# Kernel optimization log

Hardware: AMD Instinct MI355X
Metric: run time of the kernel (lower is better)

## Reference

```python
import jax, jax.numpy as jnp
import numpy as np

B, S, H, STATIC = 128, 128, 256, 2
BLOCKS = S // 2            # rotate_types = 2 for block_dim=2, allow_rot=True
DYN = 3 * BLOCKS           # dynamic channels: move / rotate_small / rotate_large


def setup_inputs() -> dict:
    key = jax.random.key(0)
    ks = jax.random.split(key, 16)
    p = lambda k, shape: (jax.random.normal(k, shape, jnp.float32) * 0.1)
    return {
        "static": jax.random.normal(ks[0], (B, STATIC + 1, S), jnp.float32),
        "dynamic": jnp.zeros((B, DYN, S), jnp.float32),
        "decoder_input": jax.random.normal(ks[1], (B, STATIC, 1), jnp.float32),
        # static/dynamic/decoder 1x1 conv encoders (weight [H, C_in], bias [H])
        "enc_s_W": p(ks[2], (H, STATIC)), "enc_s_b": p(ks[3], (H,)),
        "enc_d_W": p(ks[4], (H, DYN)),    "enc_d_b": p(ks[5], (H,)),
        "dec_W": p(ks[6], (H, STATIC)),   "dec_b": p(ks[7], (H,)),
        # single-layer GRU (torch layout: [3H, H] gates r,z,n)
        "gru_W_ih": p(ks[8], (3 * H, H)), "gru_W_hh": p(ks[9], (3 * H, H)),
        "gru_b_ih": p(ks[10], (3 * H,)),  "gru_b_hh": p(ks[11], (3 * H,)),
        # encoder attention and pointer heads: v [H], W [H, 3H]
        "attn_v": p(ks[12], (H,)), "attn_W": p(ks[13], (H, 3 * H)),
        "ptr_v": p(ks[14], (H,)),  "ptr_W": p(ks[15], (H, 3 * H)),
    }


def reference(static, dynamic, decoder_input,
              enc_s_W, enc_s_b, enc_d_W, enc_d_b, dec_W, dec_b,
              gru_W_ih, gru_W_hh, gru_b_ih, gru_b_hh,
              attn_v, attn_W, ptr_v, ptr_W):
    static_part = static[:, 1:, :]                                  # [B, STATIC, S]
    static_h = jnp.einsum('hi,bis->bhs', enc_s_W, static_part) + enc_s_b[None, :, None]
    dynamic_h = jnp.einsum('hi,bis->bhs', enc_d_W, dynamic) + enc_d_b[None, :, None]

    # initial mask from dynamic state (move + rotate feasibility)
    bn = dynamic.shape[1] // 3
    move = dynamic[:, :bn, :].sum(1)
    dyn_mask = dynamic[:, bn:2 * bn, :].sum(1) * dynamic[:, 2 * bn:3 * bn, :].sum(1) + move
    logmask = jnp.where(dyn_mask != 0, -jnp.inf, 0.0)               # log(current_mask), [B, S]

    hsz = gru_W_hh.shape[1]
    h0 = jnp.zeros((static.shape[0], hsz), static.dtype)            # GRU default zero state

    def gru_cell(x, h):
        gi = x @ gru_W_ih.T + gru_b_ih
        gh = h @ gru_W_hh.T + gru_b_hh
        ir, iz, inn = jnp.split(gi, 3, -1)
        hr, hz, hn = jnp.split(gh, 3, -1)
        r = jax.nn.sigmoid(ir + hr)
        z = jax.nn.sigmoid(iz + hz)
        n = jnp.tanh(inn + r * hn)
        return (1.0 - z) * n + z * h

    def step(carry, _):
        h_prev, dec_in = carry
        dec_h = jnp.einsum('hi,bi->bh', dec_W, dec_in[:, :, 0]) + dec_b   # decoder 1x1 conv
        h = gru_cell(dec_h, h_prev)                                       # rnn_out == new hidden
        rnn_b = jnp.broadcast_to(h[:, :, None], static_h.shape)
        hid = jnp.concatenate([static_h, dynamic_h, rnn_b], axis=1)       # [B, 3H, S]
        attn = jax.nn.softmax(
            jnp.einsum('h,bhs->bs', attn_v,
                       jnp.tanh(jnp.einsum('hk,bks->bhs', attn_W, hid))), axis=-1)
        context = jnp.einsum('bs,bhs->bh', attn, static_h)
        ctx_b = jnp.broadcast_to(context[:, :, None], static_h.shape)
        energy = jnp.concatenate([static_h, dynamic_h, ctx_b], axis=1)    # [B, 3H, S]
        logits = jnp.einsum('h,bhs->bs', ptr_v,
                            jnp.tanh(jnp.einsum('hk,bks->bhs', ptr_W, energy)))
        probs = jax.nn.softmax(logits + logmask, axis=-1)                 # [B, S]
        ptr = jnp.argmax(probs, axis=1)                                   # greedy (eval mode)
        logp = jnp.log(jnp.max(probs, axis=1))
        new_dec = jax.lax.stop_gradient(
            jnp.take_along_axis(static_part, ptr[:, None, None], axis=2))  # [B, STATIC, 1]
        return (h, new_dec), (ptr, logp)

    (_, _), (ptrs, logps) = jax.lax.scan(step, (h0, decoder_input), None,
                                         length=static_part.shape[2])
    tour_idx = ptrs.T    # [B, S]
    tour_logp = logps.T  # [B, S]
    return tour_idx, tour_logp
```

## Files before the change

kernel.cpp:

```cpp
#include <hip/hip_runtime.h>
#include <hip/hip_bf16.h>
#include <math.h>

#define BB   128
#define SS   128
#define HH   256
#define DYNN 192
#define LC   96

#define OFF_FLAG  0
#define OFF_G     64
#define OFF_G0    (OFF_G + 1536)
#define OFF_M1A   (OFF_G0 + 768)
#define OFF_CA    (OFF_M1A + 512)
#define OFF_M1P   (OFF_CA + 256)
#define OFF_CP    (OFF_M1P + 512)
#define OFF_M3P   (OFF_CP + 256)
#define OFF_CP3   (OFF_M3P + 512)
#define OFF_LM    (OFF_CP3 + 256)
#define OFF_M2A   (OFF_LM + 16384)
#define OFF_M2P   (OFF_M2A + 49152)
#define OFF_BASEA (OFF_M2P + 49152)
#define OFF_BASEP (OFF_BASEA + 4194304)
#define OFF_END   (OFF_BASEP + 4194304)

__device__ __forceinline__ float tanh_fast(float x) {
    float e = __builtin_amdgcn_exp2f(x * 2.885390081777927f);
    return 1.0f - 2.0f * __builtin_amdgcn_rcpf(e + 1.0f);
}

__device__ __forceinline__ void ybar(int* cnt, bool arrive, int target) {
    if (arrive && (threadIdx.x & 63) == 0)
        __hip_atomic_fetch_add(cnt, 1, __ATOMIC_RELEASE, __HIP_MEMORY_SCOPE_WORKGROUP);
    while (__hip_atomic_load(cnt, __ATOMIC_ACQUIRE, __HIP_MEMORY_SCOPE_WORKGROUP) < target)
        __builtin_amdgcn_s_sleep(1);
}

__global__ void k1_logmask(const float* __restrict__ dyn, float* __restrict__ lm,
                           int* __restrict__ flag) {
    int g = blockIdx.x * 256 + threadIdx.x;
    if (g >= BB * SS) return;
    int b = g >> 7, s = g & 127;
    const float* p = dyn + (size_t)b * DYNN * SS + s;
    float mv = 0.f, m1 = 0.f, m2 = 0.f;
    bool nz = false;
    for (int i = 0; i < 64; ++i)        { float v = p[(size_t)i * SS]; mv += v; nz |= (v != 0.f); }
    for (int i = 64; i < 128; ++i)      { float v = p[(size_t)i * SS]; m1 += v; nz |= (v != 0.f); }
    for (int i = 128; i < 192; ++i)     { float v = p[(size_t)i * SS]; m2 += v; nz |= (v != 0.f); }
    float dm = m1 * m2 + mv;
    lm[g] = (dm != 0.f) ? -__builtin_inff() : 0.f;
    if (nz) atomicOr(flag, 1);
}

__global__ void k0a_folds(const float* __restrict__ Wih, const float* __restrict__ bih,
                          const float* __restrict__ dW,  const float* __restrict__ db,
                          const float* __restrict__ aW,  const float* __restrict__ pW,
                          const float* __restrict__ esW, const float* __restrict__ esb,
                          const float* __restrict__ edb, float* __restrict__ wsf) {
    int idx = blockIdx.x * 256 + threadIdx.x;
    float* G   = wsf + OFF_G;
    float* g0  = wsf + OFF_G0;
    float* M1a = wsf + OFF_M1A;
    float* ca  = wsf + OFF_CA;
    float* M1p = wsf + OFF_M1P;
    float* cp  = wsf + OFF_CP;
    float* M3p = wsf + OFF_M3P;
    float* cp3 = wsf + OFF_CP3;
    if (idx < 1536) {
        int r = idx >> 1, j = idx & 1;
        float a = 0.f;
        for (int k = 0; k < 256; ++k) a += Wih[r * 256 + k] * dW[k * 2 + j];
        G[idx] = a;
    } else if (idx < 2304) {
        int r = idx - 1536;
        float a = 0.f;
        for (int k = 0; k < 256; ++k) a += Wih[r * 256 + k] * db[k];
        g0[r] = a + bih[r];
    } else if (idx < 2816) {
        int t = idx - 2304; int h = t >> 1, j = t & 1;
        float a = 0.f;
        for (int k = 0; k < 256; ++k) a += aW[h * 768 + k] * esW[k * 2 + j];
        M1a[t] = a;
    } else if (idx < 3072) {
        int h = idx - 2816;
        float a = 0.f, b2 = 0.f;
        for (int k = 0; k < 256; ++k) a  += aW[h * 768 + k]       * esb[k];
        for (int k = 0; k < 256; ++k) b2 += aW[h * 768 + 256 + k] * edb[k];
        ca[h] = a + b2;
    } else if (idx < 3584) {
        int t = idx - 3072; int h = t >> 1, j = t & 1;
        float a = 0.f;
        for (int k = 0; k < 256; ++k) a += pW[h * 768 + k] * esW[k * 2 + j];
        M1p[t] = a;
    } else if (idx < 3840) {
        int h = idx - 3584;
        float a = 0.f, b2 = 0.f;
        for (int k = 0; k < 256; ++k) a  += pW[h * 768 + k]       * esb[k];
        for (int k = 0; k < 256; ++k) b2 += pW[h * 768 + 256 + k] * edb[k];
        cp[h] = a + b2;
    } else if (idx < 4352) {
        int t = idx - 3840; int h = t >> 1, j = t & 1;
        float a = 0.f;
        for (int k = 0; k < 256; ++k) a += pW[h * 768 + 512 + k] * esW[k * 2 + j];
        M3p[t] = a;
    } else if (idx < 4608) {
        int h = idx - 4352;
        float a = 0.f;
        for (int k = 0; k < 256; ++k) a += pW[h * 768 + 512 + k] * esb[k];
        cp3[h] = a;
    }
}

__global__ void k0b_m2(const float* __restrict__ aW, const float* __restrict__ pW,
                       const float* __restrict__ edW, float* __restrict__ wsf,
                       const int* __restrict__ flag) {
    if (*flag == 0) return;
    int idx = blockIdx.x * 256 + threadIdx.x;
    if (idx >= 2 * 49152) return;
    int which = idx / 49152;
    int t = idx % 49152;
    int h = t / DYNN, i = t % DYNN;
    const float* W = which ? pW : aW;
    float a = 0.f;
    for (int k = 0; k < 256; ++k) a += W[h * 768 + 256 + k] * edW[k * DYNN + i];
    wsf[(which ? OFF_M2P : OFF_M2A) + t] = a;
}

__global__ void k2_bases(const float* __restrict__ stat, const float* __restrict__ dyn,
                         float* __restrict__ wsf, const int* __restrict__ flag) {
    if (*flag == 0) return;
    __shared__ float col[DYNN];
    __shared__ float s01[2];
    const float* M1a = wsf + OFF_M1A; const float* ca  = wsf + OFF_CA;
    const float* M1p = wsf + OFF_M1P; const float* cp  = wsf + OFF_CP;
    const float* M2a = wsf + OFF_M2A; const float* M2p = wsf + OFF_M2P;
    float* basea = wsf + OFF_BASEA;   float* basep = wsf + OFF_BASEP;
    for (int pair = blockIdx.x; pair < BB * SS; pair += gridDim.x) {
        int b = pair >> 7, s = pair & 127;
        if (threadIdx.x < DYNN) col[threadIdx.x] = dyn[((size_t)b * DYNN + threadIdx.x) * SS + s];
        if (threadIdx.x == DYNN) {
            s01[0] = stat[((size_t)b * 3 + 1) * SS + s];
            s01[1] = stat[((size_t)b * 3 + 2) * SS + s];
        }
        __syncthreads();
        int h = threadIdx.x;
        float aa = fmaf(M1a[h * 2], s01[0], fmaf(M1a[h * 2 + 1], s01[1], ca[h]));
        float pp = fmaf(M1p[h * 2], s01[0], fmaf(M1p[h * 2 + 1], s01[1], cp[h]));
        for (int i = 0; i < DYNN; ++i) {
            aa = fmaf(M2a[h * DYNN + i], col[i], aa);
            pp = fmaf(M2p[h * DYNN + i], col[i], pp);
        }
        basea[((size_t)b * SS + s) * HH + h] = aa;
        basep[((size_t)b * SS + s) * HH + h] = pp;
        __syncthreads();
    }
}

__global__ __launch_bounds__(1024) void k3_seq(
    const float* __restrict__ stat, const float* __restrict__ dec_inp,
    const float* __restrict__ Whh, const float* __restrict__ bhh_g,
    const float* __restrict__ aW, const float* __restrict__ av,
    const float* __restrict__ pv, const float* __restrict__ wsf,
    int allow_general, float* __restrict__ out) {
    const int b = blockIdx.x;
    const int tid = threadIdx.x;

    __shared__ float sh_whh[LC][256];
    __shared__ float sh_gh[768], sh_hv[256], sh_t1[256], sh_a[128];
    __shared__ float sh_sp0[128], sh_sp1[128], sh_lm[128];
    __shared__ float4 qa1[64], qa2[64], qva[64];
    __shared__ float4 qp1[64], qp2[64], qvp[64];
    __shared__ float sh_M3p[512];
    __shared__ float sh_ca[256], sh_cp[256], sh_cp3[256];
    __shared__ float sh_G[1536], sh_g0[768], sh_bhh[768];
    __shared__ float sh_va[256], sh_vp[256];
    __shared__ float sh_scal[4];
    __shared__ int ycnt;

    const float* G_   = wsf + OFF_G;   const float* g0_  = wsf + OFF_G0;
    const float* M1a_ = wsf + OFF_M1A; const float* ca_  = wsf + OFF_CA;
    const float* M1p_ = wsf + OFF_M1P; const float* cp_  = wsf + OFF_CP;
    const float* M3p_ = wsf + OFF_M3P; const float* cp3_ = wsf + OFF_CP3;
    const float* lm_  = wsf + OFF_LM;
    const float* basea = wsf + OFF_BASEA;
    const float* basep = wsf + OFF_BASEP;
    const int* flag = (const int*)wsf;

    {
        float4* dst = (float4*)&sh_whh[0][0];
        const float4* src = (const float4*)Whh;
        for (int i = tid; i < LC * 64; i += 1024) dst[i] = src[i];
    }
    for (int i = tid; i < 1536; i += 1024) sh_G[i] = G_[i];
    for (int i = tid; i < 768; i += 1024) {
        sh_g0[i] = g0_[i];
        float bv = bhh_g[i];
        sh_bhh[i] = bv;
        sh_gh[i] = bv;
    }
    for (int i = tid; i < 512; i += 1024) sh_M3p[i] = M3p_[i];
    for (int i = tid; i < 256; i += 1024) {
        sh_ca[i] = ca_[i]; sh_cp[i] = cp_[i]; sh_cp3[i] = cp3_[i];
        sh_va[i] = av[i];  sh_vp[i] = pv[i];  sh_hv[i] = 0.f;
    }
    for (int i = tid; i < 128; i += 1024) {
        sh_sp0[i] = stat[((size_t)b * 3 + 1) * SS + i];
        sh_sp1[i] = stat[((size_t)b * 3 + 2) * SS + i];
        sh_lm[i]  = lm_[b * SS + i];
    }
    if (tid < 64) {
        int q = tid;
        qa1[q] = make_float4(M1a_[(4*q+0)*2], M1a_[(4*q+1)*2], M1a_[(4*q+2)*2], M1a_[(4*q+3)*2]);
        qa2[q] = make_float4(M1a_[(4*q+0)*2+1], M1a_[(4*q+1)*2+1], M1a_[(4*q+2)*2+1], M1a_[(4*q+3)*2+1]);
        qva[q] = make_float4(av[4*q+0], av[4*q+1], av[4*q+2], av[4*q+3]);
    } else if (tid < 128) {
        int q = tid - 64;
        qp1[q] = make_float4(M1p_[(4*q+0)*2], M1p_[(4*q+1)*2], M1p_[(4*q+2)*2], M1p_[(4*q+3)*2]);
        qp2[q] = make_float4(M1p_[(4*q+0)*2+1], M1p_[(4*q+1)*2+1], M1p_[(4*q+2)*2+1], M1p_[(4*q+3)*2+1]);
        qvp[q] = make_float4(pv[4*q+0], pv[4*q+1], pv[4*q+2], pv[4*q+3]);
    }
    if (tid == 0) {
        sh_scal[0] = dec_inp[b * 2 + 0];
        sh_scal[1] = dec_inp[b * 2 + 1];
        ycnt = 0;
    }
    const bool dz = (!allow_general) || (*flag == 0);
    __syncthreads();

    for (int t = 0; t < SS; ++t) {
        if (tid < 256) {
            int k = tid;
            float d0 = sh_scal[0], d1 = sh_scal[1];
            float gr = fmaf(sh_G[k * 2],          d0, fmaf(sh_G[k * 2 + 1],          d1, sh_g0[k]));
            float gz = fmaf(sh_G[(k + 256) * 2],  d0, fmaf(sh_G[(k + 256) * 2 + 1],  d1, sh_g0[k + 256]));
            float gn = fmaf(sh_G[(k + 512) * 2],  d0, fmaf(sh_G[(k + 512) * 2 + 1],  d1, sh_g0[k + 512]));
            float r = 1.f / (1.f + expf(-(gr + sh_gh[k])));
            float z = 1.f / (1.f + expf(-(gz + sh_gh[k + 256])));
            float n = tanhf(gn + r * sh_gh[k + 512]);
            sh_hv[k] = (1.f - z) * n + z * sh_hv[k];
        }
        __syncthreads();

        if (tid < 512) {
            if (t + 1 < SS) {
                const int xg = tid >> 4, xj = tid & 15;
                float4 hx0 = ((const float4*)sh_hv)[xj];
                float4 hx1 = ((const float4*)sh_hv)[xj + 16];
                float4 hx2 = ((const float4*)sh_hv)[xj + 32];
                float4 hx3 = ((const float4*)sh_hv)[xj + 48];
                #pragma unroll
                for (int k = 0; k < 3; ++k) {
                    int r = xg + 32 * k;
                    const float4* Wr = (const float4*)&sh_whh[r][0];
                    float4 w0 = Wr[xj];
                    float4 w1 = Wr[xj + 16];
                    float4 w2 = Wr[xj + 32];
                    float4 w3 = Wr[xj + 48];
                    float acc = 0.f;
                    acc = fmaf(w0.x, hx0.x, fmaf(w0.y, hx0.y, fmaf(w0.z, hx0.z, fmaf(w0.w, hx0.w, acc))));
                    acc = fmaf(w1.x, hx1.x, fmaf(w1.y, hx1.y, fmaf(w1.z, hx1.z, fmaf(w1.w, hx1.w, acc))));
                    acc = fmaf(w2.x, hx2.x, fmaf(w2.y, hx2.y, fmaf(w2.z, hx2.z, fmaf(w2.w, hx2.w, acc))));
                    acc = fmaf(w3.x, hx3.x, fmaf(w3.y, hx3.y, fmaf(w3.z, hx3.z, fmaf(w3.w, hx3.w, acc))));
                    acc += __shfl_xor(acc, 1, 16); acc += __shfl_xor(acc, 2, 16);
                    acc += __shfl_xor(acc, 4, 16); acc += __shfl_xor(acc, 8, 16);
                    if (xj == 0) sh_gh[r] = acc + sh_bhh[r];
                }
                #pragma unroll 2
                for (int k = 3; k < 24; ++k) {
                    int r = xg + 32 * k;
                    const float4* Wr = (const float4*)(Whh + (size_t)r * 256);
                    float4 w0 = Wr[xj];
                    float4 w1 = Wr[xj + 16];
                    float4 w2 = Wr[xj + 32];
                    float4 w3 = Wr[xj + 48];
                    float acc = 0.f;
                    acc = fmaf(w0.x, hx0.x, fmaf(w0.y, hx0.y, fmaf(w0.z, hx0.z, fmaf(w0.w, hx0.w, acc))));
                    acc = fmaf(w1.x, hx1.x, fmaf(w1.y, hx1.y, fmaf(w1.z, hx1.z, fmaf(w1.w, hx1.w, acc))));
                    acc = fmaf(w2.x, hx2.x, fmaf(w2.y, hx2.y, fmaf(w2.z, hx2.z, fmaf(w2.w, hx2.w, acc))));
                    acc = fmaf(w3.x, hx3.x, fmaf(w3.y, hx3.y, fmaf(w3.z, hx3.z, fmaf(w3.w, hx3.w, acc))));
                    acc += __shfl_xor(acc, 1, 16); acc += __shfl_xor(acc, 2, 16);
                    acc += __shfl_xor(acc, 4, 16); acc += __shfl_xor(acc, 8, 16);
                    if (xj == 0) sh_gh[r] = acc + sh_bhh[r];
                }
            }
        } else {
            const int yt = tid - 512;
            const int ybase = t * 25;

            {
                const int yq = yt >> 4, yj = yt & 15;
                float4 hx0 = ((const float4*)sh_hv)[yj];
                float4 hx1 = ((const float4*)sh_hv)[yj + 16];
                float4 hx2 = ((const float4*)sh_hv)[yj + 32];
                float4 hx3 = ((const float4*)sh_hv)[yj + 48];
                #pragma unroll 2
                for (int k = 0; k < 8; ++k) {
                    int r = yq + 32 * k;
                    const float4* Wr = (const float4*)(aW + (size_t)r * 768 + 512);
                    float4 w0 = Wr[yj];
                    float4 w1 = Wr[yj + 16];
                    float4 w2 = Wr[yj + 32];
                    float4 w3 = Wr[yj + 48];
                    float acc = 0.f;
                    acc = fmaf(w0.x, hx0.x, fmaf(w0.y, hx0.y, fmaf(w0.z, hx0.z, fmaf(w0.w, hx0.w, acc))));
                    acc = fmaf(w1.x, hx1.x, fmaf(w1.y, hx1.y, fmaf(w1.z, hx1.z, fmaf(w1.w, hx1.w, acc))));
                    acc = fmaf(w2.x, hx2.x, fmaf(w2.y, hx2.y, fmaf(w2.z, hx2.z, fmaf(w2.w, hx2.w, acc))));
                    acc = fmaf(w3.x, hx3.x, fmaf(w3.y, hx3.y, fmaf(w3.z, hx3.z, fmaf(w3.w, hx3.w, acc))));
                    acc += __shfl_xor(acc, 1, 16); acc += __shfl_xor(acc, 2, 16);
                    acc += __shfl_xor(acc, 4, 16); acc += __shfl_xor(acc, 8, 16);
                    if (yj == 0) sh_t1[r] = acc + (dz ? sh_ca[r] : 0.f);
                }
            }
            ybar(&ycnt, true, ybase + 8);

            {
                int s = yt >> 2, g = yt & 3;
                float acc = 0.f;
                if (dz) {
                    float s0 = sh_sp0[s], s1 = sh_sp1[s];
                    #pragma unroll 4
                    for (int q = g; q < 64; q += 4) {
                        float4 A1 = qa1[q], A2 = qa2[q], V = qva[q];
                        float4 T = ((const float4*)sh_t1)[q];
                        acc = fmaf(V.x, tanh_fast(fmaf(A1.x, s0, fmaf(A2.x, s1, T.x))), acc);
                        acc = fmaf(V.y, tanh_fast(fmaf(A1.y, s0, fmaf(A2.y, s1, T.y))), acc);
                        acc = fmaf(V.z, tanh_fast(fmaf(A1.z, s0, fmaf(A2.z, s1, T.z))), acc);
                        acc = fmaf(V.w, tanh_fast(fmaf(A1.w, s0, fmaf(A2.w, s1, T.w))), acc);
                    }
                } else {
                    const float* bb = basea + ((size_t)b * SS + s) * HH;
                    #pragma unroll 8
                    for (int i = g; i < 256; i += 4)
                        acc = fmaf(sh_va[i], tanh_fast(bb[i] + sh_t1[i]), acc);
                }
                acc += __shfl_xor(acc, 1, 4); acc += __shfl_xor(acc, 2, 4);
                if (g == 0) sh_a[s] = acc;
            }
            ybar(&ycnt, true, ybase + 16);

            if (yt < 64) {
                int lane = yt;
                float v0 = sh_a[lane], v1 = sh_a[lane + 64];
                float m = fmaxf(v0, v1);
                for (int msk = 1; msk < 64; msk <<= 1) m = fmaxf(m, __shfl_xor(m, msk, 64));
                float e0 = expf(v0 - m), e1 = expf(v1 - m);
                float S = e0 + e1;
                float c0 = e0 * sh_sp0[lane] + e1 * sh_sp0[lane + 64];
                float c1 = e0 * sh_sp1[lane] + e1 * sh_sp1[lane + 64];
                for (int msk = 1; msk < 64; msk <<= 1) {
                    S  += __shfl_xor(S,  msk, 64);
                    c0 += __shfl_xor(c0, msk, 64);
                    c1 += __shfl_xor(c1, msk, 64);
                }
                float C0 = c0 / S, C1 = c1 / S;
                #pragma unroll
                for (int q = 0; q < 4; ++q) {
                    int k2 = lane + 64 * q;
                    float v = fmaf(sh_M3p[k2 * 2], C0, fmaf(sh_M3p[k2 * 2 + 1], C1, sh_cp3[k2]));
                    sh_t1[k2] = v + (dz ? sh_cp[k2] : 0.f);
                }
                ybar(&ycnt, true, ybase + 17);
            } else {
                ybar(&ycnt, false, ybase + 17);
            }

            {
                int s = yt >> 2, g = yt & 3;
                float acc = 0.f;
                if (dz) {
                    float s0 = sh_sp0[s], s1 = sh_sp1[s];
                    #pragma unroll 4
                    for (int q = g; q < 64; q += 4) {
                        float4 A1 = qp1[q], A2 = qp2[q], V = qvp[q];
                        float4 T = ((const float4*)sh_t1)[q];
                        acc = fmaf(V.x, tanh_fast(fmaf(A1.x, s0, fmaf(A2.x, s1, T.x))), acc);
                        acc = fmaf(V.y, tanh_fast(fmaf(A1.y, s0, fmaf(A2.y, s1, T.y))), acc);
                        acc = fmaf(V.z, tanh_fast(fmaf(A1.z, s0, fmaf(A2.z, s1, T.z))), acc);
                        acc = fmaf(V.w, tanh_fast(fmaf(A1.w, s0, fmaf(A2.w, s1, T.w))), acc);
                    }
                } else {
                    const float* bb = basep + ((size_t)b * SS + s) * HH;
                    #pragma unroll 8
                    for (int i = g; i < 256; i += 4)
                        acc = fmaf(sh_vp[i], tanh_fast(bb[i] + sh_t1[i]), acc);
                }
                acc += __shfl_xor(acc, 1, 4); acc += __shfl_xor(acc, 2, 4);
                if (g == 0) sh_a[s] = acc;
            }
            ybar(&ycnt, true, ybase + 25);

            if (yt < 64) {
                int lane = yt;
                float l0 = sh_a[lane] + sh_lm[lane];
                float l1 = sh_a[lane + 64] + sh_lm[lane + 64];
                float v; int idx;
                if (l0 >= l1) { v = l0; idx = lane; } else { v = l1; idx = lane + 64; }
                for (int msk = 1; msk < 64; msk <<= 1) {
                    float ov = __shfl_xor(v, msk, 64);
                    int   oi = __shfl_xor(idx, msk, 64);
                    if (ov > v || (ov == v && oi < idx)) { v = ov; idx = oi; }
                }
                float S = expf(l0 - v) + expf(l1 - v);
                for (int msk = 1; msk < 64; msk <<= 1) S += __shfl_xor(S, msk, 64);
                if (lane == 0) {
                    out[b * SS + t] = (float)idx;
                    out[BB * SS + b * SS + t] = -logf(S);
                    sh_scal[0] = sh_sp0[idx];
                    sh_scal[1] = sh_sp1[idx];
                }
            }
        }
        __syncthreads();
    }
}

extern "C" void kernel_launch(void* const* d_in, const int* in_sizes, int n_in,
                              void* d_out, int out_size, void* d_ws, size_t ws_size,
                              hipStream_t stream) {
    const float* stat  = (const float*)d_in[0];
    const float* dyn   = (const float*)d_in[1];
    const float* decin = (const float*)d_in[2];
    const float* esW   = (const float*)d_in[3];
    const float* esb   = (const float*)d_in[4];
    const float* edW   = (const float*)d_in[5];
    const float* edb   = (const float*)d_in[6];
    const float* dW    = (const float*)d_in[7];
    const float* db    = (const float*)d_in[8];
    const float* Wih   = (const float*)d_in[9];
    const float* Whh   = (const float*)d_in[10];
    const float* bih   = (const float*)d_in[11];
    const float* bhh   = (const float*)d_in[12];
    const float* av    = (const float*)d_in[13];
    const float* aW    = (const float*)d_in[14];
    const float* pv    = (const float*)d_in[15];
    const float* pW    = (const float*)d_in[16];
    float* wsf = (float*)d_ws;
    int* flag  = (int*)d_ws;
    float* out = (float*)d_out;

    int allow_general = (ws_size >= (size_t)OFF_END * 4) ? 1 : 0;

    hipMemsetAsync(d_ws, 0, 256, stream);
    hipLaunchKernelGGL(k1_logmask, dim3(64), dim3(256), 0, stream, dyn, wsf + OFF_LM, flag);
    hipLaunchKernelGGL(k0a_folds, dim3(18), dim3(256), 0, stream,
                       Wih, bih, dW, db, aW, pW, esW, esb, edb, wsf);
    if (allow_general) {
        hipLaunchKernelGGL(k0b_m2, dim3(384), dim3(256), 0, stream, aW, pW, edW, wsf, flag);
        hipLaunchKernelGGL(k2_bases, dim3(256), dim3(256), 0, stream, stat, dyn, wsf, flag);
    }
    hipLaunchKernelGGL(k3_seq, dim3(128), dim3(1024), 0, stream,
                       stat, decin, Whh, bhh, aW, av, pv, wsf, allow_general, out);
}
```

Measured before the change: 1.816 ms.

## Stream GRU and attention weights through double-buffered LDS via async global_load_lds

Replaces the partially LDS-resident W_hh (96 rows cached, the rest read from global) with a per-wave double-buffered stream. Each wave asynchronously copies 4-row chunks of W_hh, and of the hidden slice of attn_W, straight into LDS with global_load_lds while it computes on the previous chunk. Rows are now assigned to waves in contiguous blocks of 96 (GRU) or 32 (attention) instead of being strided. The G table moves from LDS to global reads so the new buffers fit. This aims to hide global-load latency in the sequential matvecs, but it re-streams all weights every step, relies on hand-placed s_waitcnt ordering, and issues wrap-around prefetches that are never consumed.

Result: slower. 2.346 ms (+29.2%).

```diff
diff --git a/kernel.cpp b/kernel.cpp
--- a/kernel.cpp
+++ b/kernel.cpp
@@ -6,7 +6,6 @@
 #define SS   128
 #define HH   256
 #define DYNN 192
-#define LC   96
 
 #define OFF_FLAG  0
 #define OFF_G     64
@@ -27,6 +26,13 @@
 __device__ __forceinline__ float tanh_fast(float x) {
     float e = __builtin_amdgcn_exp2f(x * 2.885390081777927f);
     return 1.0f - 2.0f * __builtin_amdgcn_rcpf(e + 1.0f);
+}
+
+__device__ __forceinline__ void gload_lds16(const float* g, float* l) {
+    __builtin_amdgcn_global_load_lds(
+        (const __attribute__((address_space(1))) void*)(g),
+        (__attribute__((address_space(3))) void*)(l),
+        16, 0, 0);
 }
 
 __device__ __forceinline__ void ybar(int* cnt, bool arrive, int target) {
@@ -165,14 +171,15 @@
     const int b = blockIdx.x;
     const int tid = threadIdx.x;
 
-    __shared__ float sh_whh[LC][256];
+    __shared__ float sh_xs[8 * 2 * 4 * 256];
+    __shared__ float sh_ys[8 * 2 * 4 * 256];
     __shared__ float sh_gh[768], sh_hv[256], sh_t1[256], sh_a[128];
     __shared__ float sh_sp0[128], sh_sp1[128], sh_lm[128];
     __shared__ float4 qa1[64], qa2[64], qva[64];
     __shared__ float4 qp1[64], qp2[64], qvp[64];
     __shared__ float sh_M3p[512];
     __shared__ float sh_ca[256], sh_cp[256], sh_cp3[256];
-    __shared__ float sh_G[1536], sh_g0[768], sh_bhh[768];
+    __shared__ float sh_g0[768], sh_bhh[768];
     __shared__ float sh_va[256], sh_vp[256];
     __shared__ float sh_scal[4];
     __shared__ int ycnt;
@@ -186,12 +193,6 @@
     const float* basep = wsf + OFF_BASEP;
     const int* flag = (const int*)wsf;
 
-    {
-        float4* dst = (float4*)&sh_whh[0][0];
-        const float4* src = (const float4*)Whh;
-        for (int i = tid; i < LC * 64; i += 1024) dst[i] = src[i];
-    }
-    for (int i = tid; i < 1536; i += 1024) sh_G[i] = G_[i];
     for (int i = tid; i < 768; i += 1024) {
         sh_g0[i] = g0_[i];
         float bv = bhh_g[i];
@@ -227,13 +228,35 @@
     const bool dz = (!allow_general) || (*flag == 0);
     __syncthreads();
 
+    const int lane = tid & 63;
+    const int q4   = (lane >> 4);
+    const int xj   = lane & 15;
+
+    if (tid < 512) {
+        int w = tid >> 6;
+        float* dst = sh_xs + w * 2048;
+        int r0 = w * 96;
+        gload_lds16(Whh + (r0 + 0) * 256 + lane * 4, dst + 0);
+        gload_lds16(Whh + (r0 + 1) * 256 + lane * 4, dst + 256);
+        gload_lds16(Whh + (r0 + 2) * 256 + lane * 4, dst + 512);
+        gload_lds16(Whh + (r0 + 3) * 256 + lane * 4, dst + 768);
+    } else {
+        int yw = (tid - 512) >> 6;
+        float* dst = sh_ys + yw * 2048;
+        int r0 = yw * 32;
+        gload_lds16(aW + (size_t)(r0 + 0) * 768 + 512 + lane * 4, dst + 0);
+        gload_lds16(aW + (size_t)(r0 + 1) * 768 + 512 + lane * 4, dst + 256);
+        gload_lds16(aW + (size_t)(r0 + 2) * 768 + 512 + lane * 4, dst + 512);
+        gload_lds16(aW + (size_t)(r0 + 3) * 768 + 512 + lane * 4, dst + 768);
+    }
+
     for (int t = 0; t < SS; ++t) {
         if (tid < 256) {
             int k = tid;
             float d0 = sh_scal[0], d1 = sh_scal[1];
-            float gr = fmaf(sh_G[k * 2],          d0, fmaf(sh_G[k * 2 + 1],          d1, sh_g0[k]));
-            float gz = fmaf(sh_G[(k + 256) * 2],  d0, fmaf(sh_G[(k + 256) * 2 + 1],  d1, sh_g0[k + 256]));
-            float gn = fmaf(sh_G[(k + 512) * 2],  d0, fmaf(sh_G[(k + 512) * 2 + 1],  d1, sh_g0[k + 512]));
+            float gr = fmaf(G_[k * 2],          d0, fmaf(G_[k * 2 + 1],          d1, sh_g0[k]));
+            float gz = fmaf(G_[(k + 256) * 2],  d0, fmaf(G_[(k + 256) * 2 + 1],  d1, sh_g0[k + 256]));
+            float gn = fmaf(G_[(k + 512) * 2],  d0, fmaf(G_[(k + 512) * 2 + 1],  d1, sh_g0[k + 512]));
             float r = 1.f / (1.f + expf(-(gr + sh_gh[k])));
             float z = 1.f / (1.f + expf(-(gz + sh_gh[k + 256])));
             float n = tanhf(gn + r * sh_gh[k + 512]);
@@ -243,15 +266,26 @@
 
         if (tid < 512) {
             if (t + 1 < SS) {
-                const int xg = tid >> 4, xj = tid & 15;
+                const int w = tid >> 6;
+                float* wbuf = sh_xs + w * 2048;
+                const int rbase = w * 96;
                 float4 hx0 = ((const float4*)sh_hv)[xj];
                 float4 hx1 = ((const float4*)sh_hv)[xj + 16];
                 float4 hx2 = ((const float4*)sh_hv)[xj + 32];
                 float4 hx3 = ((const float4*)sh_hv)[xj + 48];
-                #pragma unroll
-                for (int k = 0; k < 3; ++k) {
-                    int r = xg + 32 * k;
-                    const float4* Wr = (const float4*)&sh_whh[r][0];
+                for (int c = 0; c < 24; ++c) {
+                    {
+                        int cc = (c + 1 < 24) ? (c + 1) : 0;
+                        int crow = rbase + cc * 4;
+                        float* dst = wbuf + ((c + 1) & 1) * 1024;
+                        gload_lds16(Whh + (crow + 0) * 256 + lane * 4, dst + 0);
+                        gload_lds16(Whh + (crow + 1) * 256 + lane * 4, dst + 256);
+                        gload_lds16(Whh + (crow + 2) * 256 + lane * 4, dst + 512);
+                        gload_lds16(Whh + (crow + 3) * 256 + lane * 4, dst + 768);
+                    }
+                    asm volatile("s_waitcnt vmcnt(4)" ::: "memory");
+                    __builtin_amdgcn_sched_barrier(0);
+                    const float4* Wr = (const float4*)(wbuf + (c & 1) * 1024 + q4 * 256);
                     float4 w0 = Wr[xj];
                     float4 w1 = Wr[xj + 16];
                     float4 w2 = Wr[xj + 32];
@@ -263,12 +297,37 @@
                     acc = fmaf(w3.x, hx3.x, fmaf(w3.y, hx3.y, fmaf(w3.z, hx3.z, fmaf(w3.w, hx3.w, acc))));
                     acc += __shfl_xor(acc, 1, 16); acc += __shfl_xor(acc, 2, 16);
                     acc += __shfl_xor(acc, 4, 16); acc += __shfl_xor(acc, 8, 16);
-                    if (xj == 0) sh_gh[r] = acc + sh_bhh[r];
-                }
-                #pragma unroll 2
-                for (int k = 3; k < 24; ++k) {
-                    int r = xg + 32 * k;
-                    const float4* Wr = (const float4*)(Whh + (size_t)r * 256);
+                    if (xj == 0) {
+                        int r = rbase + c * 4 + q4;
+                        sh_gh[r] = acc + sh_bhh[r];
+                    }
+                }
+            }
+        } else {
+            const int yt = tid - 512;
+            const int ybase = t * 25;
+
+            {
+                const int yw = yt >> 6;
+                float* ybuf = sh_ys + yw * 2048;
+                const int rbase = yw * 32;
+                float4 hx0 = ((const float4*)sh_hv)[xj];
+                float4 hx1 = ((const float4*)sh_hv)[xj + 16];
+                float4 hx2 = ((const float4*)sh_hv)[xj + 32];
+                float4 hx3 = ((const float4*)sh_hv)[xj + 48];
+                for (int c = 0; c < 8; ++c) {
+                    {
+                        int cc = (c + 1) & 7;
+                        int crow = rbase + cc * 4;
+                        float* dst = ybuf + ((c + 1) & 1) * 1024;
+                        gload_lds16(aW + (size_t)(crow + 0) * 768 + 512 + lane * 4, dst + 0);
+                        gload_lds16(aW + (size_t)(crow + 1) * 768 + 512 + lane * 4, dst + 256);
+                        gload_lds16(aW + (size_t)(crow + 2) * 768 + 512 + lane * 4, dst + 512);
+                        gload_lds16(aW + (size_t)(crow + 3) * 768 + 512 + lane * 4, dst + 768);
+                    }
+                    asm volatile("s_waitcnt vmcnt(4)" ::: "memory");
+                    __builtin_amdgcn_sched_barrier(0);
+                    const float4* Wr = (const float4*)(ybuf + (c & 1) * 1024 + q4 * 256);
                     float4 w0 = Wr[xj];
                     float4 w1 = Wr[xj + 16];
                     float4 w2 = Wr[xj + 32];
@@ -280,35 +339,10 @@
                     acc = fmaf(w3.x, hx3.x, fmaf(w3.y, hx3.y, fmaf(w3.z, hx3.z, fmaf(w3.w, hx3.w, acc))));
                     acc += __shfl_xor(acc, 1, 16); acc += __shfl_xor(acc, 2, 16);
                     acc += __shfl_xor(acc, 4, 16); acc += __shfl_xor(acc, 8, 16);
-                    if (xj == 0) sh_gh[r] = acc + sh_bhh[r];
-                }
-            }
-        } else {
-            const int yt = tid - 512;
-            const int ybase = t * 25;
-
-            {
-                const int yq = yt >> 4, yj = yt & 15;
-                float4 hx0 = ((const float4*)sh_hv)[yj];
-                float4 hx1 = ((const float4*)sh_hv)[yj + 16];
-                float4 hx2 = ((const float4*)sh_hv)[yj + 32];
-                float4 hx3 = ((const float4*)sh_hv)[yj + 48];
-                #pragma unroll 2
-                for (int k = 0; k < 8; ++k) {
-                    int r = yq + 32 * k;
-                    const float4* Wr = (const float4*)(aW + (size_t)r * 768 + 512);
-                    float4 w0 = Wr[yj];
-                    float4 w1 = Wr[yj + 16];
-                    float4 w2 = Wr[yj + 32];
-                    float4 w3 = Wr[yj + 48];
-                    float acc = 0.f;
-                    acc = fmaf(w0.x, hx0.x, fmaf(w0.y, hx0.y, fmaf(w0.z, hx0.z, fmaf(w0.w, hx0.w, acc))));
-                    acc = fmaf(w1.x, hx1.x, fmaf(w1.y, hx1.y, fmaf(w1.z, hx1.z, fmaf(w1.w, hx1.w, acc))));
-                    acc = fmaf(w2.x, hx2.x, fmaf(w2.y, hx2.y, fmaf(w2.z, hx2.z, fmaf(w2.w, hx2.w, acc))));
-                    acc = fmaf(w3.x, hx3.x, fmaf(w3.y, hx3.y, fmaf(w3.z, hx3.z, fmaf(w3.w, hx3.w, acc))));
-                    acc += __shfl_xor(acc, 1, 16); acc += __shfl_xor(acc, 2, 16);
-                    acc += __shfl_xor(acc, 4, 16); acc += __shfl_xor(acc, 8, 16);
-                    if (yj == 0) sh_t1[r] = acc + (dz ? sh_ca[r] : 0.f);
+                    if (xj == 0) {
+                        int r = rbase + c * 4 + q4;
+                        sh_t1[r] = acc + (dz ? sh_ca[r] : 0.f);
+                    }
                 }
             }
             ybar(&ycnt, true, ybase + 8);
@@ -339,14 +373,14 @@
             ybar(&ycnt, true, ybase + 16);
 
             if (yt < 64) {
-                int lane = yt;
-                float v0 = sh_a[lane], v1 = sh_a[lane + 64];
+                int ln = yt;
+                float v0 = sh_a[ln], v1 = sh_a[ln + 64];
                 float m = fmaxf(v0, v1);
                 for (int msk = 1; msk < 64; msk <<= 1) m = fmaxf(m, __shfl_xor(m, msk, 64));
                 float e0 = expf(v0 - m), e1 = expf(v1 - m);
                 float S = e0 + e1;
-                float c0 = e0 * sh_sp0[lane] + e1 * sh_sp0[lane + 64];
-                float c1 = e0 * sh_sp1[lane] + e1 * sh_sp1[lane + 64];
+                float c0 = e0 * sh_sp0[ln] + e1 * sh_sp0[ln + 64];
+                float c1 = e0 * sh_sp1[ln] + e1 * sh_sp1[ln + 64];
                 for (int msk = 1; msk < 64; msk <<= 1) {
                     S  += __shfl_xor(S,  msk, 64);
                     c0 += __shfl_xor(c0, msk, 64);
@@ -355,7 +389,7 @@
                 float C0 = c0 / S, C1 = c1 / S;
                 #pragma unroll
                 for (int q = 0; q < 4; ++q) {
-                    int k2 = lane + 64 * q;
+                    int k2 = ln + 64 * q;
                     float v = fmaf(sh_M3p[k2 * 2], C0, fmaf(sh_M3p[k2 * 2 + 1], C1, sh_cp3[k2]));
                     sh_t1[k2] = v + (dz ? sh_cp[k2] : 0.f);
                 }
@@ -390,11 +424,11 @@
             ybar(&ycnt, true, ybase + 25);
 
             if (yt < 64) {
-                int lane = yt;
-                float l0 = sh_a[lane] + sh_lm[lane];
-                float l1 = sh_a[lane + 64] + sh_lm[lane + 64];
+                int ln = yt;
+                float l0 = sh_a[ln] + sh_lm[ln];
+                float l1 = sh_a[ln + 64] + sh_lm[ln + 64];
                 float v; int idx;
-                if (l0 >= l1) { v = l0; idx = lane; } else { v = l1; idx = lane + 64; }
+                if (l0 >= l1) { v = l0; idx = ln; } else { v = l1; idx = ln + 64; }
                 for (int msk = 1; msk < 64; msk <<= 1) {
                     float ov = __shfl_xor(v, msk, 64);
                     int   oi = __shfl_xor(idx, msk, 64);
@@ -402,7 +436,7 @@
                 }
                 float S = expf(l0 - v) + expf(l1 - v);
                 for (int msk = 1; msk < 64; msk <<= 1) S += __shfl_xor(S, msk, 64);
-                if (lane == 0) {
+                if (ln == 0) {
                     out[b * SS + t] = (float)idx;
                     out[BB * SS + b * SS + t] = -logf(S);
                     sh_scal[0] = sh_sp0[idx];
```

## Halve sequential block to 512 threads and cache weight rows in registers

Applied to the files above, without the earlier changes.

The per-batch sequential kernel now runs with 512 threads instead of 1024. Each GRU-side thread keeps 8 rows of W_hh in registers and each attention-side thread keeps 8 rows of the attention weight slice, so fewer rows are fetched from global memory on every step. Rows 128-223 of W_hh are served from shared memory and the rest still come from global memory. The shared va/vp vectors are dropped, the fallback base paths are vectorised, and the per-thread work in the scoring loops doubles. The large register arrays risk spills or lower occupancy, and the halved thread count lengthens each thread's serial work per step.

After: 2.772 ms. 52.6% more time.

```diff
diff --git a/kernel.cpp b/kernel.cpp
--- a/kernel.cpp
+++ b/kernel.cpp
@@ -6,7 +6,6 @@
 #define SS   128
 #define HH   256
 #define DYNN 192
-#define LC   96
 
 #define OFF_FLAG  0
 #define OFF_G     64
@@ -156,7 +155,7 @@
     }
 }
 
-__global__ __launch_bounds__(1024) void k3_seq(
+__global__ __launch_bounds__(512, 2) void k3_seq(
     const float* __restrict__ stat, const float* __restrict__ dec_inp,
     const float* __restrict__ Whh, const float* __restrict__ bhh_g,
     const float* __restrict__ aW, const float* __restrict__ av,
@@ -165,7 +164,7 @@
     const int b = blockIdx.x;
     const int tid = threadIdx.x;
 
-    __shared__ float sh_whh[LC][256];
+    __shared__ float sh_whh[96][256];
     __shared__ float sh_gh[768], sh_hv[256], sh_t1[256], sh_a[128];
     __shared__ float sh_sp0[128], sh_sp1[128], sh_lm[128];
     __shared__ float4 qa1[64], qa2[64], qva[64];
@@ -173,7 +172,6 @@
     __shared__ float sh_M3p[512];
     __shared__ float sh_ca[256], sh_cp[256], sh_cp3[256];
     __shared__ float sh_G[1536], sh_g0[768], sh_bhh[768];
-    __shared__ float sh_va[256], sh_vp[256];
     __shared__ float sh_scal[4];
     __shared__ int ycnt;
 
@@ -188,22 +186,22 @@
 
     {
         float4* dst = (float4*)&sh_whh[0][0];
-        const float4* src = (const float4*)Whh;
-        for (int i = tid; i < LC * 64; i += 1024) dst[i] = src[i];
-    }
-    for (int i = tid; i < 1536; i += 1024) sh_G[i] = G_[i];
-    for (int i = tid; i < 768; i += 1024) {
+        const float4* src = (const float4*)(Whh + 128 * 256);
+        for (int i = tid; i < 96 * 64; i += 512) dst[i] = src[i];
+    }
+    for (int i = tid; i < 1536; i += 512) sh_G[i] = G_[i];
+    for (int i = tid; i < 768; i += 512) {
         sh_g0[i] = g0_[i];
         float bv = bhh_g[i];
         sh_bhh[i] = bv;
         sh_gh[i] = bv;
     }
-    for (int i = tid; i < 512; i += 1024) sh_M3p[i] = M3p_[i];
-    for (int i = tid; i < 256; i += 1024) {
+    for (int i = tid; i < 512; i += 512) sh_M3p[i] = M3p_[i];
+    for (int i = tid; i < 256; i += 512) {
         sh_ca[i] = ca_[i]; sh_cp[i] = cp_[i]; sh_cp3[i] = cp3_[i];
-        sh_va[i] = av[i];  sh_vp[i] = pv[i];  sh_hv[i] = 0.f;
-    }
-    for (int i = tid; i < 128; i += 1024) {
+        sh_hv[i] = 0.f;
+    }
+    for (int i = tid; i < 128; i += 512) {
         sh_sp0[i] = stat[((size_t)b * 3 + 1) * SS + i];
         sh_sp1[i] = stat[((size_t)b * 3 + 2) * SS + i];
         sh_lm[i]  = lm_[b * SS + i];
@@ -225,7 +223,35 @@
         ycnt = 0;
     }
     const bool dz = (!allow_general) || (*flag == 0);
+
+    const int grp = (tid & 255) >> 4;
+    const int gj  = tid & 15;
+    float4 cw[8][4];
+    float4 ca3[8][4];
+    if (tid < 256) {
+        #pragma unroll
+        for (int k = 0; k < 8; ++k) {
+            const float4* Wr = (const float4*)(Whh + (size_t)(grp + 16 * k) * 256);
+            cw[k][0] = Wr[gj]; cw[k][1] = Wr[gj + 16]; cw[k][2] = Wr[gj + 32]; cw[k][3] = Wr[gj + 48];
+        }
+    } else {
+        #pragma unroll
+        for (int k = 0; k < 8; ++k) {
+            const float4* Wr = (const float4*)(aW + (size_t)(grp + 16 * k) * 768 + 512);
+            ca3[k][0] = Wr[gj]; ca3[k][1] = Wr[gj + 16]; ca3[k][2] = Wr[gj + 32]; ca3[k][3] = Wr[gj + 48];
+        }
+    }
     __syncthreads();
+
+#define ROW_DOT(Wr)                                                                              \
+    float4 w0 = (Wr)[0], w1 = (Wr)[1], w2 = (Wr)[2], w3 = (Wr)[3];                               \
+    float acc = 0.f;                                                                             \
+    acc = fmaf(w0.x, hx0.x, fmaf(w0.y, hx0.y, fmaf(w0.z, hx0.z, fmaf(w0.w, hx0.w, acc))));       \
+    acc = fmaf(w1.x, hx1.x, fmaf(w1.y, hx1.y, fmaf(w1.z, hx1.z, fmaf(w1.w, hx1.w, acc))));       \
+    acc = fmaf(w2.x, hx2.x, fmaf(w2.y, hx2.y, fmaf(w2.z, hx2.z, fmaf(w2.w, hx2.w, acc))));       \
+    acc = fmaf(w3.x, hx3.x, fmaf(w3.y, hx3.y, fmaf(w3.z, hx3.z, fmaf(w3.w, hx3.w, acc))));       \
+    acc += __shfl_xor(acc, 1, 16); acc += __shfl_xor(acc, 2, 16);                                \
+    acc += __shfl_xor(acc, 4, 16); acc += __shfl_xor(acc, 8, 16);
 
     for (int t = 0; t < SS; ++t) {
         if (tid < 256) {
@@ -241,85 +267,68 @@
         }
         __syncthreads();
 
-        if (tid < 512) {
+        if (tid < 256) {
             if (t + 1 < SS) {
-                const int xg = tid >> 4, xj = tid & 15;
-                float4 hx0 = ((const float4*)sh_hv)[xj];
-                float4 hx1 = ((const float4*)sh_hv)[xj + 16];
-                float4 hx2 = ((const float4*)sh_hv)[xj + 32];
-                float4 hx3 = ((const float4*)sh_hv)[xj + 48];
+                float4 hx0 = ((const float4*)sh_hv)[gj];
+                float4 hx1 = ((const float4*)sh_hv)[gj + 16];
+                float4 hx2 = ((const float4*)sh_hv)[gj + 32];
+                float4 hx3 = ((const float4*)sh_hv)[gj + 48];
                 #pragma unroll
-                for (int k = 0; k < 3; ++k) {
-                    int r = xg + 32 * k;
-                    const float4* Wr = (const float4*)&sh_whh[r][0];
-                    float4 w0 = Wr[xj];
-                    float4 w1 = Wr[xj + 16];
-                    float4 w2 = Wr[xj + 32];
-                    float4 w3 = Wr[xj + 48];
-                    float acc = 0.f;
-                    acc = fmaf(w0.x, hx0.x, fmaf(w0.y, hx0.y, fmaf(w0.z, hx0.z, fmaf(w0.w, hx0.w, acc))));
-                    acc = fmaf(w1.x, hx1.x, fmaf(w1.y, hx1.y, fmaf(w1.z, hx1.z, fmaf(w1.w, hx1.w, acc))));
-                    acc = fmaf(w2.x, hx2.x, fmaf(w2.y, hx2.y, fmaf(w2.z, hx2.z, fmaf(w2.w, hx2.w, acc))));
-                    acc = fmaf(w3.x, hx3.x, fmaf(w3.y, hx3.y, fmaf(w3.z, hx3.z, fmaf(w3.w, hx3.w, acc))));
-                    acc += __shfl_xor(acc, 1, 16); acc += __shfl_xor(acc, 2, 16);
-                    acc += __shfl_xor(acc, 4, 16); acc += __shfl_xor(acc, 8, 16);
-                    if (xj == 0) sh_gh[r] = acc + sh_bhh[r];
+                for (int k = 0; k < 8; ++k) {
+                    const float4* Wr = &cw[k][0];
+                    ROW_DOT(Wr)
+                    if (gj == 0) { int r = grp + 16 * k; sh_gh[r] = acc + sh_bhh[r]; }
+                }
+                #pragma unroll
+                for (int k = 8; k < 14; ++k) {
+                    int r = grp + 16 * k;
+                    const float4* Wb = (const float4*)&sh_whh[r - 128][0];
+                    const float4 Wr[4] = { Wb[gj], Wb[gj + 16], Wb[gj + 32], Wb[gj + 48] };
+                    ROW_DOT(Wr)
+                    if (gj == 0) sh_gh[r] = acc + sh_bhh[r];
                 }
                 #pragma unroll 2
-                for (int k = 3; k < 24; ++k) {
-                    int r = xg + 32 * k;
-                    const float4* Wr = (const float4*)(Whh + (size_t)r * 256);
-                    float4 w0 = Wr[xj];
-                    float4 w1 = Wr[xj + 16];
-                    float4 w2 = Wr[xj + 32];
-                    float4 w3 = Wr[xj + 48];
-                    float acc = 0.f;
-                    acc = fmaf(w0.x, hx0.x, fmaf(w0.y, hx0.y, fmaf(w0.z, hx0.z, fmaf(w0.w, hx0.w, acc))));
-                    acc = fmaf(w1.x, hx1.x, fmaf(w1.y, hx1.y, fmaf(w1.z, hx1.z, fmaf(w1.w, hx1.w, acc))));
-                    acc = fmaf(w2.x, hx2.x, fmaf(w2.y, hx2.y, fmaf(w2.z, hx2.z, fmaf(w2.w, hx2.w, acc))));
-                    acc = fmaf(w3.x, hx3.x, fmaf(w3.y, hx3.y, fmaf(w3.z, hx3.z, fmaf(w3.w, hx3.w, acc))));
-                    acc += __shfl_xor(acc, 1, 16); acc += __shfl_xor(acc, 2, 16);
-                    acc += __shfl_xor(acc, 4, 16); acc += __shfl_xor(acc, 8, 16);
-                    if (xj == 0) sh_gh[r] = acc + sh_bhh[r];
+                for (int k = 14; k < 48; ++k) {
+                    int r = grp + 16 * k;
+                    const float4* Wb = (const float4*)(Whh + (size_t)r * 256);
+                    const float4 Wr[4] = { Wb[gj], Wb[gj + 16], Wb[gj + 32], Wb[gj + 48] };
+                    ROW_DOT(Wr)
+                    if (gj == 0) sh_gh[r] = acc + sh_bhh[r];
                 }
             }
         } else {
-            const int yt = tid - 512;
-            const int ybase = t * 25;
+            const int yt = tid - 256;
+            const int ybase = t * 13;
 
             {
-                const int yq = yt >> 4, yj = yt & 15;
-                float4 hx0 = ((const float4*)sh_hv)[yj];
-                float4 hx1 = ((const float4*)sh_hv)[yj + 16];
-                float4 hx2 = ((const float4*)sh_hv)[yj + 32];
-                float4 hx3 = ((const float4*)sh_hv)[yj + 48];
+                float4 hx0 = ((const float4*)sh_hv)[gj];
+                float4 hx1 = ((const float4*)sh_hv)[gj + 16];
+                float4 hx2 = ((const float4*)sh_hv)[gj + 32];
+                float4 hx3 = ((const float4*)sh_hv)[gj + 48];
+                #pragma unroll
+                for (int k = 0; k < 8; ++k) {
+                    const float4* Wr = &ca3[k][0];
+                    ROW_DOT(Wr)
+                    if (gj == 0) { int r = grp + 16 * k; sh_t1[r] = acc + (dz ? sh_ca[r] : 0.f); }
+                }
                 #pragma unroll 2
-                for (int k = 0; k < 8; ++k) {
-                    int r = yq + 32 * k;
-                    const float4* Wr = (const float4*)(aW + (size_t)r * 768 + 512);
-                    float4 w0 = Wr[yj];
-                    float4 w1 = Wr[yj + 16];
-                    float4 w2 = Wr[yj + 32];
-                    float4 w3 = Wr[yj + 48];
-                    float acc = 0.f;
-                    acc = fmaf(w0.x, hx0.x, fmaf(w0.y, hx0.y, fmaf(w0.z, hx0.z, fmaf(w0.w, hx0.w, acc))));
-                    acc = fmaf(w1.x, hx1.x, fmaf(w1.y, hx1.y, fmaf(w1.z, hx1.z, fmaf(w1.w, hx1.w, acc))));
-                    acc = fmaf(w2.x, hx2.x, fmaf(w2.y, hx2.y, fmaf(w2.z, hx2.z, fmaf(w2.w, hx2.w, acc))));
-                    acc = fmaf(w3.x, hx3.x, fmaf(w3.y, hx3.y, fmaf(w3.z, hx3.z, fmaf(w3.w, hx3.w, acc))));
-                    acc += __shfl_xor(acc, 1, 16); acc += __shfl_xor(acc, 2, 16);
-                    acc += __shfl_xor(acc, 4, 16); acc += __shfl_xor(acc, 8, 16);
-                    if (yj == 0) sh_t1[r] = acc + (dz ? sh_ca[r] : 0.f);
-                }
-            }
-            ybar(&ycnt, true, ybase + 8);
+                for (int k = 8; k < 16; ++k) {
+                    int r = grp + 16 * k;
+                    const float4* Wb = (const float4*)(aW + (size_t)r * 768 + 512);
+                    const float4 Wr[4] = { Wb[gj], Wb[gj + 16], Wb[gj + 32], Wb[gj + 48] };
+                    ROW_DOT(Wr)
+                    if (gj == 0) sh_t1[r] = acc + (dz ? sh_ca[r] : 0.f);
+                }
+            }
+            ybar(&ycnt, true, ybase + 4);
 
             {
-                int s = yt >> 2, g = yt & 3;
+                int s = yt >> 1, g = yt & 1;
                 float acc = 0.f;
                 if (dz) {
                     float s0 = sh_sp0[s], s1 = sh_sp1[s];
                     #pragma unroll 4
-                    for (int q = g; q < 64; q += 4) {
+                    for (int q = g; q < 64; q += 2) {
                         float4 A1 = qa1[q], A2 = qa2[q], V = qva[q];
                         float4 T = ((const float4*)sh_t1)[q];
                         acc = fmaf(V.x, tanh_fast(fmaf(A1.x, s0, fmaf(A2.x, s1, T.x))), acc);
@@ -328,25 +337,31 @@
                         acc = fmaf(V.w, tanh_fast(fmaf(A1.w, s0, fmaf(A2.w, s1, T.w))), acc);
                     }
                 } else {
-                    const float* bb = basea + ((size_t)b * SS + s) * HH;
-                    #pragma unroll 8
-                    for (int i = g; i < 256; i += 4)
-                        acc = fmaf(sh_va[i], tanh_fast(bb[i] + sh_t1[i]), acc);
-                }
-                acc += __shfl_xor(acc, 1, 4); acc += __shfl_xor(acc, 2, 4);
+                    #pragma unroll 4
+                    for (int q = g; q < 64; q += 2) {
+                        float4 V = qva[q];
+                        float4 T = ((const float4*)sh_t1)[q];
+                        float4 B = *(const float4*)(basea + ((size_t)b * SS + s) * HH + q * 4);
+                        acc = fmaf(V.x, tanh_fast(B.x + T.x), acc);
+                        acc = fmaf(V.y, tanh_fast(B.y + T.y), acc);
+                        acc = fmaf(V.z, tanh_fast(B.z + T.z), acc);
+                        acc = fmaf(V.w, tanh_fast(B.w + T.w), acc);
+                    }
+                }
+                acc += __shfl_xor(acc, 1, 2);
                 if (g == 0) sh_a[s] = acc;
             }
-            ybar(&ycnt, true, ybase + 16);
+            ybar(&ycnt, true, ybase + 8);
 
             if (yt < 64) {
-                int lane = yt;
-                float v0 = sh_a[lane], v1 = sh_a[lane + 64];
+                int ln = yt;
+                float v0 = sh_a[ln], v1 = sh_a[ln + 64];
                 float m = fmaxf(v0, v1);
                 for (int msk = 1; msk < 64; msk <<= 1) m = fmaxf(m, __shfl_xor(m, msk, 64));
                 float e0 = expf(v0 - m), e1 = expf(v1 - m);
                 float S = e0 + e1;
-                float c0 = e0 * sh_sp0[lane] + e1 * sh_sp0[lane + 64];
-                float c1 = e0 * sh_sp1[lane] + e1 * sh_sp1[lane + 64];
+                float c0 = e0 * sh_sp0[ln] + e1 * sh_sp0[ln + 64];
+                float c1 = e0 * sh_sp1[ln] + e1 * sh_sp1[ln + 64];
                 for (int msk = 1; msk < 64; msk <<= 1) {
                     S  += __shfl_xor(S,  msk, 64);
                     c0 += __shfl_xor(c0, msk, 64);
@@ -355,22 +370,22 @@
                 float C0 = c0 / S, C1 = c1 / S;
                 #pragma unroll
                 for (int q = 0; q < 4; ++q) {
-                    int k2 = lane + 64 * q;
+                    int k2 = ln + 64 * q;
                     float v = fmaf(sh_M3p[k2 * 2], C0, fmaf(sh_M3p[k2 * 2 + 1], C1, sh_cp3[k2]));
                     sh_t1[k2] = v + (dz ? sh_cp[k2] : 0.f);
                 }
-                ybar(&ycnt, true, ybase + 17);
+                ybar(&ycnt, true, ybase + 9);
             } else {
-                ybar(&ycnt, false, ybase + 17);
+                ybar(&ycnt, false, ybase + 9);
             }
 
             {
-                int s = yt >> 2, g = yt & 3;
+                int s = yt >> 1, g = yt & 1;
                 float acc = 0.f;
                 if (dz) {
                     float s0 = sh_sp0[s], s1 = sh_sp1[s];
                     #pragma unroll 4
-                    for (int q = g; q < 64; q += 4) {
+                    for (int q = g; q < 64; q += 2) {
                         float4 A1 = qp1[q], A2 = qp2[q], V = qvp[q];
                         float4 T = ((const float4*)sh_t1)[q];
                         acc = fmaf(V.x, tanh_fast(fmaf(A1.x, s0, fmaf(A2.x, s1, T.x))), acc);
@@ -379,22 +394,28 @@
                         acc = fmaf(V.w, tanh_fast(fmaf(A1.w, s0, fmaf(A2.w, s1, T.w))), acc);
                     }
                 } else {
-                    const float* bb = basep + ((size_t)b * SS + s) * HH;
-                    #pragma unroll 8
-                    for (int i = g; i < 256; i += 4)
-                        acc = fmaf(sh_vp[i], tanh_fast(bb[i] + sh_t1[i]), acc);
-                }
-                acc += __shfl_xor(acc, 1, 4); acc += __shfl_xor(acc, 2, 4);
+                    #pragma unroll 4
+                    for (int q = g; q < 64; q += 2) {
+                        float4 V = qvp[q];
+                        float4 T = ((const float4*)sh_t1)[q];
+                        float4 B = *(const float4*)(basep + ((size_t)b * SS + s) * HH + q * 4);
+                        acc = fmaf(V.x, tanh_fast(B.x + T.x), acc);
+                        acc = fmaf(V.y, tanh_fast(B.y + T.y), acc);
+                        acc = fmaf(V.z, tanh_fast(B.z + T.z), acc);
+                        acc = fmaf(V.w, tanh_fast(B.w + T.w), acc);
+                    }
+                }
+                acc += __shfl_xor(acc, 1, 2);
                 if (g == 0) sh_a[s] = acc;
             }
-            ybar(&ycnt, true, ybase + 25);
+            ybar(&ycnt, true, ybase + 13);
 
             if (yt < 64) {
-                int lane = yt;
-                float l0 = sh_a[lane] + sh_lm[lane];
-                float l1 = sh_a[lane + 64] + sh_lm[lane + 64];
+                int ln = yt;
+                float l0 = sh_a[ln] + sh_lm[ln];
+                float l1 = sh_a[ln + 64] + sh_lm[ln + 64];
                 float v; int idx;
-                if (l0 >= l1) { v = l0; idx = lane; } else { v = l1; idx = lane + 64; }
+                if (l0 >= l1) { v = l0; idx = ln; } else { v = l1; idx = ln + 64; }
                 for (int msk = 1; msk < 64; msk <<= 1) {
                     float ov = __shfl_xor(v, msk, 64);
                     int   oi = __shfl_xor(idx, msk, 64);
@@ -402,7 +423,7 @@
                 }
                 float S = expf(l0 - v) + expf(l1 - v);
                 for (int msk = 1; msk < 64; msk <<= 1) S += __shfl_xor(S, msk, 64);
-                if (lane == 0) {
+                if (ln == 0) {
                     out[b * SS + t] = (float)idx;
                     out[BB * SS + b * SS + t] = -logf(S);
                     sh_scal[0] = sh_sp0[idx];
@@ -412,6 +433,7 @@
         }
         __syncthreads();
     }
+#undef ROW_DOT
 }
 
 extern "C" void kernel_launch(void* const* d_in, const int* in_sizes, int n_in,
@@ -448,6 +470,6 @@
         hipLaunchKernelGGL(k0b_m2, dim3(384), dim3(256), 0, stream, aW, pW, edW, wsf, flag);
         hipLaunchKernelGGL(k2_bases, dim3(256), dim3(256), 0, stream, stat, dyn, wsf, flag);
     }
-    hipLaunchKernelGGL(k3_seq, dim3(128), dim3(1024), 0, stream,
+    hipLaunchKernelGGL(k3_seq, dim3(128), dim3(512), 0, stream,
                        stat, decin, Whh, bhh, aW, av, pv, wsf, allow_general, out);
 }
```
